# Optimization experiments

Hardware: AMD Instinct MI355X
Metric: run time of the kernel (lower is better)

The kernel has to match this reference:

```python
import jax, jax.numpy as jnp
import numpy as np

B, N, DEG = 64, 512, 16        # graphs, nodes per graph, avg degree
C, HID = 10, 128               # input feat dim (== num_classes quirk), hidden
E = B * N * DEG                # total edges (fixed; pooling masks edges)


def _gcn(x, W, b, src, dst, emask, n):
    # PyG GCNConv: add self-loops, symmetric norm D^-1/2 (A+I) D^-1/2 (XW) + b
    h = x @ W
    deg = jax.ops.segment_sum(emask, dst, num_segments=n) + 1.0  # +1 self-loop
    dinv = jax.lax.rsqrt(deg)
    norm = dinv[src] * dinv[dst] * emask
    agg = jax.ops.segment_sum(h[src] * norm[:, None], dst, num_segments=n)
    return agg + h * (dinv * dinv)[:, None] + b  # self-loop term + bias


def _sag_pool(x, src, dst, emask, Wp, bp, n_per):
    # SAGPooling: score = tanh(GCN(x)); per-graph top-k (ratio=0.5); x' = x[perm]*score
    n = x.shape[0]
    score = jnp.tanh(_gcn(x, Wp, bp, src, dst, emask, n)[:, 0])
    k = n_per // 2
    vals, idx = jax.lax.top_k(score.reshape(B, n_per), k)  # [B,k]
    perm = (idx + (jnp.arange(B) * n_per)[:, None]).reshape(-1)
    xk = x[perm] * vals.reshape(-1)[:, None]
    # relabel edges; drop edges touching removed nodes via mask (fixed E)
    mapping = jnp.full((n,), -1, jnp.int32).at[perm].set(
        jnp.arange(B * k, dtype=jnp.int32))
    ns, nd = mapping[src], mapping[dst]
    nmask = emask * ((ns >= 0) & (nd >= 0)).astype(emask.dtype)
    return xk, jnp.maximum(ns, 0), jnp.maximum(nd, 0), nmask, k


def _readout(x, k):
    # global max pool || global mean pool (all kept nodes are real, no padding)
    xg = x.reshape(B, k, -1)
    return jnp.concatenate([xg.max(axis=1), xg.mean(axis=1)], axis=1)


def setup_inputs() -> dict:
    key = jax.random.key(0)
    ks = jax.random.split(key, 16)
    x = jax.random.normal(ks[0], (B * N, C), jnp.float32)
    off = jnp.repeat(jnp.arange(B, dtype=jnp.int32) * N, N * DEG)
    src = jax.random.randint(ks[1], (E,), 0, N, jnp.int32) + off
    dst = jax.random.randint(ks[2], (E,), 0, N, jnp.int32) + off
    p = lambda k, s: jax.random.normal(k, s, jnp.float32) * 0.05
    return {
        "x": x, "src": src, "dst": dst,
        "W1": p(ks[3], (C, HID)), "b1": jnp.zeros((HID,), jnp.float32),
        "W2": p(ks[4], (HID, HID)), "b2": jnp.zeros((HID,), jnp.float32),
        "W3": p(ks[5], (HID, HID)), "b3": jnp.zeros((HID,), jnp.float32),
        "Wp": p(ks[6], (HID, 1)), "bp": jnp.zeros((1,), jnp.float32),
        "L1W": p(ks[7], (2 * HID, HID)), "L1b": jnp.zeros((HID,), jnp.float32),
        "L2W": p(ks[8], (HID, HID // 2)), "L2b": jnp.zeros((HID // 2,), jnp.float32),
    }


def reference(x, src, dst, W1, b1, W2, b2, W3, b3, Wp, bp, L1W, L1b, L2W, L2b):
    emask = jnp.ones((E,), jnp.float32)
    h = jax.nn.relu(_gcn(x, W1, b1, src, dst, emask, B * N))
    h, src, dst, emask, k = _sag_pool(h, src, dst, emask, Wp, bp, N)
    x1 = _readout(h, k)
    h = jax.nn.relu(_gcn(h, W2, b2, src, dst, emask, B * k))
    h, src, dst, emask, k = _sag_pool(h, src, dst, emask, Wp, bp, k)
    x2 = _readout(h, k)
    h = jax.nn.relu(_gcn(h, W3, b3, src, dst, emask, B * k))
    h, src, dst, emask, k = _sag_pool(h, src, dst, emask, Wp, bp, k)
    x3 = _readout(h, k)
    z = x1 + x2 + x3
    z = jax.nn.relu(z @ L1W + L1b)
    # dropout inactive in eval mode
    z = jax.nn.relu(z @ L2W + L2b)
    return jax.nn.log_softmax(z, axis=1)
```

## Files before the change

### kernel.cpp

```cpp
#include <hip/hip_runtime.h>
#include <math.h>

#define BGR 64
#define N0 512
#define E_TOT (BGR*N0*16)
#define EPG 8192
#define EIT 16
#define HID 128


__global__ __launch_bounds__(512) void k_topo0(
    const int* __restrict__ s0, const int* __restrict__ d0,
    int2* __restrict__ edges, int* __restrict__ cnt, int* __restrict__ rowptr,
    float* __restrict__ dinv, int2* __restrict__ csr){
  __shared__ int   deg[512];
  __shared__ int   sb[512];
  __shared__ int   cur[512];
  __shared__ float dl[512];
  int g = (blockIdx.x & 7)*8 + (blockIdx.x >> 3);
  int t = threadIdx.x;
  int gbase = g*N0, ebase = g*EPG;
  deg[t] = 0;
  __syncthreads();
  int2 ebuf[EIT];
  #pragma unroll
  for (int it = 0; it < EIT; it++){
    int i = ebase + it*512 + t;
    int2 e = make_int2(s0[i], d0[i]);
    ebuf[it] = e;
    edges[i] = e;
    atomicAdd(&deg[e.y - gbase], 1);
  }
  __syncthreads();
  int vdeg = deg[t];
  sb[t] = vdeg; __syncthreads();
  for (int off = 1; off < 512; off <<= 1){
    int add = (t >= off) ? sb[t-off] : 0;
    __syncthreads(); sb[t] += add; __syncthreads();
  }
  int excl = sb[t] - vdeg;
  rowptr[gbase + t] = ebase + excl;
  cnt[gbase + t] = vdeg;
  cur[t] = excl;
  float dv = rsqrtf((float)vdeg + 1.f);
  dl[t] = dv;
  dinv[gbase + t] = dv;
  __syncthreads();
  #pragma unroll
  for (int it = 0; it < EIT; it++){
    int2 e = ebuf[it];
    int sl = e.x - gbase, dc = e.y - gbase;
    int pos = atomicAdd(&cur[dc], 1);
    csr[ebase + pos] = make_int2(e.x, __float_as_int(dl[sl]*dl[dc]));
  }
}

__global__ __launch_bounds__(512) void k_l1_fused(
    const float* __restrict__ x, const float* __restrict__ W1,
    const int2* __restrict__ csr, const int* __restrict__ rowptr,
    const int* __restrict__ cnt, const float* __restrict__ dinv,
    const float* __restrict__ b1, const float* __restrict__ Wp,
    float4* __restrict__ gout4, float* __restrict__ hp_part){
  extern __shared__ float hl[];
  int b = blockIdx.x;
  int xcd = b & 7, idx = b >> 3;
  int graph = xcd*8 + (idx >> 3);
  int sub = idx & 7;
  int qf = sub >> 1, half = sub & 1;
  int t = threadIdx.x;
  int gbase = graph*N0;
  int fp = t & 31;
  int f = qf*32 + fp;
  float wcol[10];
  #pragma unroll
  for (int k = 0; k < 10; k++) wcol[k] = W1[k*HID + f];
  for (int n = t >> 5; n < N0; n += 16){
    const float* xr = x + (gbase + n)*10;
    float acc = 0.f;
    #pragma unroll
    for (int k = 0; k < 10; k++) acc += xr[k]*wcol[k];
    hl[n*32 + fp] = acc;
  }
  __syncthreads();
  const float4* hl4 = (const float4*)hl;
  int l = t & 7, grp = t >> 3;
  float4 bb = ((const float4*)b1)[qf*8 + l];
  float4 wp = ((const float4*)Wp)[qf*8 + l];
  int n0 = half*256;
  for (int nl = n0 + grp; nl < n0 + 256; nl += 64){
    int node = gbase + nl;
    int start = rowptr[node], c = cnt[node];
    float4 acc = make_float4(0.f,0.f,0.f,0.f);
    int j = 0;
    for (; j + 4 <= c; j += 4){
      int2 e0 = csr[start+j],   e1 = csr[start+j+1];
      int2 e2 = csr[start+j+2], e3 = csr[start+j+3];
      float4 h0 = hl4[(e0.x - gbase)*8 + l];
      float4 h1 = hl4[(e1.x - gbase)*8 + l];
      float4 h2 = hl4[(e2.x - gbase)*8 + l];
      float4 h3 = hl4[(e3.x - gbase)*8 + l];
      float w0 = __int_as_float(e0.y), w1 = __int_as_float(e1.y);
      float w2 = __int_as_float(e2.y), w3 = __int_as_float(e3.y);
      acc.x += w0*h0.x + w1*h1.x + w2*h2.x + w3*h3.x;
      acc.y += w0*h0.y + w1*h1.y + w2*h2.y + w3*h3.y;
      acc.z += w0*h0.z + w1*h1.z + w2*h2.z + w3*h3.z;
      acc.w += w0*h0.w + w1*h1.w + w2*h2.w + w3*h3.w;
    }
    for (; j < c; j++){
      int2 e = csr[start + j];
      float wgt = __int_as_float(e.y);
      float4 hv = hl4[(e.x - gbase)*8 + l];
      acc.x += wgt*hv.x; acc.y += wgt*hv.y; acc.z += wgt*hv.z; acc.w += wgt*hv.w;
    }
    float di = dinv[node], dd = di*di;
    float4 hs = hl4[nl*8 + l];
    float4 v;
    v.x = fmaxf(acc.x + hs.x*dd + bb.x, 0.f);
    v.y = fmaxf(acc.y + hs.y*dd + bb.y, 0.f);
    v.z = fmaxf(acc.z + hs.z*dd + bb.z, 0.f);
    v.w = fmaxf(acc.w + hs.w*dd + bb.w, 0.f);
    gout4[node*32 + qf*8 + l] = v;
    float contrib = v.x*wp.x + v.y*wp.y + v.z*wp.z + v.w*wp.w;
    #pragma unroll
    for (int off = 4; off; off >>= 1) contrib += __shfl_down(contrib, off, 8);
    if (l == 0) hp_part[qf*32768 + node] = contrib;
  }
}

__global__ void k_gemm16(const float* __restrict__ x, const float* __restrict__ W,
                         float* __restrict__ out, int nper){
  __shared__ float xr[16][HID];
  int b = blockIdx.x;
  int xcd = b & 7, idx = b >> 3, bpg = nper >> 4;
  int graph = xcd*8 + idx / bpg;
  int base = graph*nper + (idx % bpg)*16;
  int f = threadIdx.x;
  #pragma unroll
  for (int nd = 0; nd < 16; nd++) xr[nd][f] = x[(base+nd)*HID + f];
  __syncthreads();
  float acc[16];
  #pragma unroll
  for (int nd = 0; nd < 16; nd++) acc[nd] = 0.f;
  for (int i = 0; i < HID; i++){
    float wv = W[i*HID + f];
    #pragma unroll
    for (int nd = 0; nd < 16; nd++) acc[nd] += xr[nd][i]*wv;
  }
  #pragma unroll
  for (int nd = 0; nd < 16; nd++) out[(base+nd)*HID + f] = acc[nd];
}

__global__ __launch_bounds__(256) void k_gcn_gather(
    const float4* __restrict__ h4, const int2* __restrict__ csr,
    const int* __restrict__ rowptr, const int* __restrict__ cnt,
    const float* __restrict__ dinv, const float4* __restrict__ bias4,
    const float4* __restrict__ Wp4, float4* __restrict__ out4,
    float* __restrict__ hp, int nper){
  int b = blockIdx.x;
  int xcd = b & 7, idx = b >> 3, bpg = nper >> 3;
  int graph = xcd*8 + idx / bpg;
  int node = graph*nper + (idx % bpg)*8 + (threadIdx.x >> 5);
  int l = threadIdx.x & 31;
  int start = rowptr[node], c = cnt[node];
  float4 acc = make_float4(0.f, 0.f, 0.f, 0.f);
  int j = 0;
  for (; j + 4 <= c; j += 4){
    int2 e0 = csr[start+j],   e1 = csr[start+j+1];
    int2 e2 = csr[start+j+2], e3 = csr[start+j+3];
    float4 h0 = h4[e0.x*32 + l];
    float4 h1 = h4[e1.x*32 + l];
    float4 h2 = h4[e2.x*32 + l];
    float4 h3 = h4[e3.x*32 + l];
    float w0 = __int_as_float(e0.y), w1 = __int_as_float(e1.y);
    float w2 = __int_as_float(e2.y), w3 = __int_as_float(e3.y);
    acc.x += w0*h0.x + w1*h1.x + w2*h2.x + w3*h3.x;
    acc.y += w0*h0.y + w1*h1.y + w2*h2.y + w3*h3.y;
    acc.z += w0*h0.z + w1*h1.z + w2*h2.z + w3*h3.z;
    acc.w += w0*h0.w + w1*h1.w + w2*h2.w + w3*h3.w;
  }
  for (; j < c; j++){
    int2 e = csr[start + j];
    float wgt = __int_as_float(e.y);
    float4 hv = h4[e.x*32 + l];
    acc.x += wgt*hv.x; acc.y += wgt*hv.y; acc.z += wgt*hv.z; acc.w += wgt*hv.w;
  }
  float di = dinv[node], dd = di*di;
  float4 hs = h4[node*32 + l];
  float4 bb = bias4[l];
  float4 v;
  v.x = fmaxf(acc.x + hs.x*dd + bb.x, 0.f);
  v.y = fmaxf(acc.y + hs.y*dd + bb.y, 0.f);
  v.z = fmaxf(acc.z + hs.z*dd + bb.z, 0.f);
  v.w = fmaxf(acc.w + hs.w*dd + bb.w, 0.f);
  out4[node*32 + l] = v;
  float4 wp = Wp4[l];
  float contrib = v.x*wp.x + v.y*wp.y + v.z*wp.z + v.w*wp.w;
  #pragma unroll
  for (int off = 16; off; off >>= 1) contrib += __shfl_down(contrib, off, 32);
  if (l == 0) hp[node] = contrib;
}

__global__ __launch_bounds__(512) void k_mega(
    const float4* __restrict__ gout4, const float* __restrict__ hp_part,
    int l1flag, const float* __restrict__ hp,
    int2* __restrict__ csr, int* __restrict__ rowptr, int* __restrict__ cnt,
    float* __restrict__ dinv, const float* __restrict__ bp,
    int2* __restrict__ edges, float4* __restrict__ xpool4,
    float* __restrict__ z, int nper, int lastlev,
    const float* __restrict__ L1W, const float* __restrict__ L1b,
    const float* __restrict__ L2W, const float* __restrict__ L2b,
    float* __restrict__ out){
  __shared__ float sv[512];
  __shared__ int   si[512];
  __shared__ float hpl[512];
  __shared__ int   map[512];
  __shared__ int   sb[512];
  __shared__ int   cur[256];
  __shared__ float dl[256];
  __shared__ float4 pmx[16][32];
  __shared__ float4 psm[16][32];
  __shared__ float zr[256];
  __shared__ float h1[128];
  __shared__ float h2[64];
  __shared__ float red[2];
  int g = (blockIdx.x & 7)*8 + (blockIdx.x >> 3);
  int t = threadIdx.x;
  int k = nper >> 1;
  int gbase = g*nper, ebase = g*EPG, gb2 = g*k;
  bool act = t < nper;
  if (act){
    int node = gbase + t;
    hpl[t] = l1flag ? (hp_part[node] + hp_part[32768 + node] +
                       hp_part[65536 + node] + hp_part[98304 + node])
                    : hp[node];
  }
  __syncthreads();
  float v = 0.f; int idx = t;
  if (act){
    int start = rowptr[gbase + t], c = cnt[gbase + t];
    float a = 0.f;
    int j = 0;
    for (; j + 4 <= c; j += 4){
      int2 e0 = csr[start+j],   e1 = csr[start+j+1];
      int2 e2 = csr[start+j+2], e3 = csr[start+j+3];
      a += __int_as_float(e0.y)*hpl[e0.x - gbase]
         + __int_as_float(e1.y)*hpl[e1.x - gbase]
         + __int_as_float(e2.y)*hpl[e2.x - gbase]
         + __int_as_float(e3.y)*hpl[e3.x - gbase];
    }
    for (; j < c; j++){
      int2 e = csr[start + j];
      a += __int_as_float(e.y)*hpl[e.x - gbase];
    }
    float di = dinv[gbase + t];
    v = tanhf(a + hpl[t]*di*di + bp[0]);
  }
  for (int kk = 2; kk <= nper; kk <<= 1){
    for (int jj = kk >> 1; jj > 0; jj >>= 1){
      if (jj >= 64){
        if (act){ sv[t] = v; si[t] = idx; }
        __syncthreads();
        if (act){
          int p = t ^ jj;
          float pv = sv[p]; int pi = si[p];
          bool amLower = (t & jj) == 0;
          bool dirDesc = (t & kk) == 0;
          bool betterMine = (v > pv) || (v == pv && idx < pi);
          if ((amLower == dirDesc) != betterMine){ v = pv; idx = pi; }
        }
        __syncthreads();
      } else if (act){
        float pv = __shfl_xor(v, jj);
        int   pi = __shfl_xor(idx, jj);
        bool amLower = (t & jj) == 0;
        bool dirDesc = (t & kk) == 0;
        bool betterMine = (v > pv) || (v == pv && idx < pi);
        if ((amLower == dirDesc) != betterMine){ v = pv; idx = pi; }
      }
    }
  }
  if (act){ sv[t] = v; si[t] = idx; }
  __syncthreads();
  int l = t & 31, j0 = t >> 5;
  float4 mx = make_float4(-INFINITY,-INFINITY,-INFINITY,-INFINITY);
  float4 sm = make_float4(0.f,0.f,0.f,0.f);
  for (int j = j0; j < k; j += 16){
    float val = sv[j]; int row = si[j];
    float4 hv = gout4[(gbase + row)*32 + l];
    float4 o = make_float4(hv.x*val, hv.y*val, hv.z*val, hv.w*val);
    if (!lastlev) xpool4[(gb2 + j)*32 + l] = o;
    mx.x = fmaxf(mx.x, o.x); mx.y = fmaxf(mx.y, o.y);
    mx.z = fmaxf(mx.z, o.z); mx.w = fmaxf(mx.w, o.w);
    sm.x += o.x; sm.y += o.y; sm.z += o.z; sm.w += o.w;
  }
  pmx[j0][l] = mx; psm[j0][l] = sm;
  __syncthreads();
  if (t < 32){
    float4 M = pmx[0][t], S = psm[0][t];
    #pragma unroll
    for (int q = 1; q < 16; q++){
      float4 m2 = pmx[q][t], s2 = psm[q][t];
      M.x = fmaxf(M.x, m2.x); M.y = fmaxf(M.y, m2.y);
      M.z = fmaxf(M.z, m2.z); M.w = fmaxf(M.w, m2.w);
      S.x += s2.x; S.y += s2.y; S.z += s2.z; S.w += s2.w;
    }
    float ki = 1.f/(float)k;
    float* zp = z + g*256;
    if (l1flag){
      zp[t*4+0] = M.x; zp[t*4+1] = M.y; zp[t*4+2] = M.z; zp[t*4+3] = M.w;
      zp[128+t*4+0] = S.x*ki; zp[128+t*4+1] = S.y*ki;
      zp[128+t*4+2] = S.z*ki; zp[128+t*4+3] = S.w*ki;
    } else if (!lastlev){
      zp[t*4+0] += M.x; zp[t*4+1] += M.y; zp[t*4+2] += M.z; zp[t*4+3] += M.w;
      zp[128+t*4+0] += S.x*ki; zp[128+t*4+1] += S.y*ki;
      zp[128+t*4+2] += S.z*ki; zp[128+t*4+3] += S.w*ki;
    } else {
      zr[t*4+0] = zp[t*4+0] + M.x; zr[t*4+1] = zp[t*4+1] + M.y;
      zr[t*4+2] = zp[t*4+2] + M.z; zr[t*4+3] = zp[t*4+3] + M.w;
      zr[128+t*4+0] = zp[128+t*4+0] + S.x*ki;
      zr[128+t*4+1] = zp[128+t*4+1] + S.y*ki;
      zr[128+t*4+2] = zp[128+t*4+2] + S.z*ki;
      zr[128+t*4+3] = zp[128+t*4+3] + S.w*ki;
    }
  }
  if (lastlev){
    __syncthreads();
    if (t < 128){
      float a = L1b[t];
      for (int i = 0; i < 256; i++) a += zr[i]*L1W[i*128 + t];
      h1[t] = fmaxf(a, 0.f);
    }
    __syncthreads();
    if (t < 64){
      float a = L2b[t];
      for (int i = 0; i < 128; i++) a += h1[i]*L2W[i*64 + t];
      h2[t] = fmaxf(a, 0.f);
    }
    __syncthreads();
    if (t == 0){
      float mxv = -INFINITY;
      for (int i = 0; i < 64; i++) mxv = fmaxf(mxv, h2[i]);
      float s = 0.f;
      for (int i = 0; i < 64; i++) s += expf(h2[i] - mxv);
      red[0] = mxv; red[1] = logf(s);
    }
    __syncthreads();
    if (t < 64) out[g*64 + t] = h2[t] - red[0] - red[1];
    return;
  }
  if (act) map[t] = -1;
  if (t < k) sb[t] = 0;
  __syncthreads();
  if (t < k) map[si[t]] = t;
  __syncthreads();
  int2 ebuf[EIT];
  #pragma unroll
  for (int it = 0; it < EIT; it++){
    int i = ebase + it*512 + t;
    int2 e = edges[i];
    int2 ne = make_int2(-1, 0);
    if (e.x >= 0){
      int ns = map[e.x - gbase], nd = map[e.y - gbase];
      if (ns >= 0 && nd >= 0){
        ne = make_int2(gb2 + ns, gb2 + nd);
        atomicAdd(&sb[nd], 1);
      }
    }
    ebuf[it] = ne;
    edges[i] = ne;
  }
  __syncthreads();
  int vdeg = (t < k) ? sb[t] : 0;
  for (int off = 1; off < k; off <<= 1){
    int add = (t >= off && t < k) ? sb[t-off] : 0;
    __syncthreads();
    if (t < k) sb[t] += add;
    __syncthreads();
  }
  if (t < k){
    int excl = sb[t] - vdeg;
    rowptr[gb2 + t] = ebase + excl;
    cnt[gb2 + t] = vdeg;
    cur[t] = excl;
    float dv = rsqrtf((float)vdeg + 1.f);
    dl[t] = dv;
    dinv[gb2 + t] = dv;
  }
  __syncthreads();
  #pragma unroll
  for (int it = 0; it < EIT; it++){
    int2 e = ebuf[it];
    if (e.x >= 0){
      int sl = e.x - gb2, dc = e.y - gb2;
      int pos = atomicAdd(&cur[dc], 1);
      csr[ebase + pos] = make_int2(e.x, __float_as_int(dl[sl]*dl[dc]));
    }
  }
}

extern "C" void kernel_launch(void* const* d_in, const int* in_sizes, int n_in,
                              void* d_out, int out_size, void* d_ws, size_t ws_size,
                              hipStream_t stream){
  (void)in_sizes; (void)n_in; (void)out_size; (void)ws_size;
  const float* x0  = (const float*)d_in[0];
  const int*   s0  = (const int*)  d_in[1];
  const int*   d0  = (const int*)  d_in[2];
  const float* W1  = (const float*)d_in[3];  const float* b1 = (const float*)d_in[4];
  const float* W2  = (const float*)d_in[5];  const float* b2 = (const float*)d_in[6];
  const float* W3  = (const float*)d_in[7];  const float* b3 = (const float*)d_in[8];
  const float* Wp  = (const float*)d_in[9];  const float* bp = (const float*)d_in[10];
  const float* L1W = (const float*)d_in[11]; const float* L1b = (const float*)d_in[12];
  const float* L2W = (const float*)d_in[13]; const float* L2b = (const float*)d_in[14];
  float* out = (float*)d_out;

  float* w = (float*)d_ws;
  float* h     = w; w += 32768*HID;
  float* gout  = w; w += 32768*HID;
  float* xpA   = h    + 16384*HID;
  float* xpB   = gout + 16384*HID;
  float* xpC   = xpA;
  float* dinvv = w; w += 32768;
  float* hp    = w; w += 32768;
  float* hppt  = w; w += 4*32768;
  float* z     = w; w += BGR*256;
  int* cnt     = (int*)w; w += 32768;
  int* rowptr  = (int*)w; w += 32768;
  int2* edges  = (int2*)w; w += 2*E_TOT;
  int2* csr    = (int2*)w; w += 2*E_TOT;

  k_topo0<<<BGR, 512, 0, stream>>>(s0, d0, edges, cnt, rowptr, dinvv, csr);

  k_l1_fused<<<512, 512, 65536, stream>>>(x0, W1, csr, rowptr, cnt, dinvv,
                                          b1, Wp, (float4*)gout, hppt);
  k_mega<<<BGR, 512, 0, stream>>>((const float4*)gout, hppt, 1, hp, csr, rowptr,
                                  cnt, dinvv, bp, edges, (float4*)xpA, z, 512, 0,
                                  L1W, L1b, L2W, L2b, out);
  k_gemm16<<<16384/16, HID, 0, stream>>>(xpA, W2, h, 256);
  k_gcn_gather<<<16384/8, 256, 0, stream>>>((const float4*)h, csr, rowptr, cnt,
                                            dinvv, (const float4*)b2,
                                            (const float4*)Wp, (float4*)gout,
                                            hp, 256);
  k_mega<<<BGR, 512, 0, stream>>>((const float4*)gout, hppt, 0, hp, csr, rowptr,
                                  cnt, dinvv, bp, edges, (float4*)xpB, z, 256, 0,
                                  L1W, L1b, L2W, L2b, out);
  k_gemm16<<<8192/16, HID, 0, stream>>>(xpB, W3, h, 128);
  k_gcn_gather<<<8192/8, 256, 0, stream>>>((const float4*)h, csr, rowptr, cnt,
                                           dinvv, (const float4*)b3,
                                           (const float4*)Wp, (float4*)gout,
                                           hp, 128);
  k_mega<<<BGR, 512, 0, stream>>>((const float4*)gout, hppt, 0, hp, csr, rowptr,
                                  cnt, dinvv, bp, edges, (float4*)xpC, z, 128, 1,
                                  L1W, L1b, L2W, L2b, out);
}
```

Before: 246.0 us.

## Fuse pooled gather into GEMM, widen mega kernel, use wave-shuffle scans

The pooling kernel no longer writes the scaled pooled feature matrix. It stores only the selected indices and scores, and the following GEMM gathers rows from the previous layer's output and scales them as it loads. The mega kernel now runs 1024 threads per graph, splitting the score aggregation across several threads per node, and uses twice as many threads for the edge relabel. Both LDS Hillis-Steele prefix scans (topology and relabel) become wave-level shuffle scans with per-wave sums, which cuts barriers. The trade-offs are indirect, less coalesced loads in the GEMM and heavier register and LDS pressure from the larger blocks.

```diff
diff --git a/kernel.cpp b/kernel.cpp
--- a/kernel.cpp
+++ b/kernel.cpp
@@ -14,9 +14,9 @@
     int2* __restrict__ edges, int* __restrict__ cnt, int* __restrict__ rowptr,
     float* __restrict__ dinv, int2* __restrict__ csr){
   __shared__ int   deg[512];
-  __shared__ int   sb[512];
   __shared__ int   cur[512];
   __shared__ float dl[512];
+  __shared__ int   wsum[8];
   int g = (blockIdx.x & 7)*8 + (blockIdx.x >> 3);
   int t = threadIdx.x;
   int gbase = g*N0, ebase = g*EPG;
@@ -33,12 +33,19 @@
   }
   __syncthreads();
   int vdeg = deg[t];
-  sb[t] = vdeg; __syncthreads();
-  for (int off = 1; off < 512; off <<= 1){
-    int add = (t >= off) ? sb[t-off] : 0;
-    __syncthreads(); sb[t] += add; __syncthreads();
-  }
-  int excl = sb[t] - vdeg;
+  int lane = t & 63, wid = t >> 6;
+  int x = vdeg;
+  #pragma unroll
+  for (int off = 1; off < 64; off <<= 1){
+    int y = __shfl_up(x, off);
+    if (lane >= off) x += y;
+  }
+  if (lane == 63) wsum[wid] = x;
+  __syncthreads();
+  int prefix = 0;
+  #pragma unroll
+  for (int wj = 0; wj < 8; wj++) prefix += (wj < wid) ? wsum[wj] : 0;
+  int excl = x + prefix - vdeg;
   rowptr[gbase + t] = ebase + excl;
   cnt[gbase + t] = vdeg;
   cur[t] = excl;
@@ -127,16 +134,23 @@
   }
 }
 
-__global__ void k_gemm16(const float* __restrict__ x, const float* __restrict__ W,
-                         float* __restrict__ out, int nper){
+__global__ void k_gemm16p(const float* __restrict__ gprev,
+                          const int* __restrict__ sig,
+                          const float* __restrict__ svg,
+                          const float* __restrict__ W,
+                          float* __restrict__ out, int nprev, int nper){
   __shared__ float xr[16][HID];
   int b = blockIdx.x;
   int xcd = b & 7, idx = b >> 3, bpg = nper >> 4;
   int graph = xcd*8 + idx / bpg;
-  int base = graph*nper + (idx % bpg)*16;
+  int lb = (idx % bpg)*16;
   int f = threadIdx.x;
   #pragma unroll
-  for (int nd = 0; nd < 16; nd++) xr[nd][f] = x[(base+nd)*HID + f];
+  for (int nd = 0; nd < 16; nd++){
+    int row  = sig[graph*512 + lb + nd];
+    float val = svg[graph*512 + lb + nd];
+    xr[nd][f] = gprev[(graph*nprev + row)*HID + f] * val;
+  }
   __syncthreads();
   float acc[16];
   #pragma unroll
@@ -147,7 +161,7 @@
     for (int nd = 0; nd < 16; nd++) acc[nd] += xr[nd][i]*wv;
   }
   #pragma unroll
-  for (int nd = 0; nd < 16; nd++) out[(base+nd)*HID + f] = acc[nd];
+  for (int nd = 0; nd < 16; nd++) out[(graph*nper + lb + nd)*HID + f] = acc[nd];
 }
 
 __global__ __launch_bounds__(256) void k_gcn_gather(
@@ -200,12 +214,12 @@
   if (l == 0) hp[node] = contrib;
 }
 
-__global__ __launch_bounds__(512) void k_mega(
+__global__ __launch_bounds__(1024) void k_mega(
     const float4* __restrict__ gout4, const float* __restrict__ hp_part,
     int l1flag, const float* __restrict__ hp,
     int2* __restrict__ csr, int* __restrict__ rowptr, int* __restrict__ cnt,
     float* __restrict__ dinv, const float* __restrict__ bp,
-    int2* __restrict__ edges, float4* __restrict__ xpool4,
+    int2* __restrict__ edges, int* __restrict__ sig, float* __restrict__ svg,
     float* __restrict__ z, int nper, int lastlev,
     const float* __restrict__ L1W, const float* __restrict__ L1b,
     const float* __restrict__ L2W, const float* __restrict__ L2b,
@@ -213,10 +227,12 @@
   __shared__ float sv[512];
   __shared__ int   si[512];
   __shared__ float hpl[512];
-  __shared__ int   map[512];
+  __shared__ float spart[1024];
+  __shared__ int   map_[512];
   __shared__ int   sb[512];
   __shared__ int   cur[256];
   __shared__ float dl[256];
+  __shared__ int   wsum[4];
   __shared__ float4 pmx[16][32];
   __shared__ float4 psm[16][32];
   __shared__ float zr[256];
@@ -227,7 +243,10 @@
   int t = threadIdx.x;
   int k = nper >> 1;
   int gbase = g*nper, ebase = g*EPG, gb2 = g*k;
+  int SPL = 1024/nper;
+  int n = t & (nper-1), p = t / nper;
   bool act = t < nper;
+
   if (act){
     int node = gbase + t;
     hpl[t] = l1flag ? (hp_part[node] + hp_part[32768 + node] +
@@ -235,23 +254,21 @@
                     : hp[node];
   }
   __syncthreads();
+  {
+    int start = rowptr[gbase + n], c = cnt[gbase + n];
+    int lo = (c*p)/SPL, hi = (c*(p+1))/SPL;
+    float a = 0.f;
+    for (int j = lo; j < hi; j++){
+      int2 e = csr[start + j];
+      a += __int_as_float(e.y)*hpl[e.x - gbase];
+    }
+    spart[t] = a;
+  }
+  __syncthreads();
   float v = 0.f; int idx = t;
   if (act){
-    int start = rowptr[gbase + t], c = cnt[gbase + t];
     float a = 0.f;
-    int j = 0;
-    for (; j + 4 <= c; j += 4){
-      int2 e0 = csr[start+j],   e1 = csr[start+j+1];
-      int2 e2 = csr[start+j+2], e3 = csr[start+j+3];
-      a += __int_as_float(e0.y)*hpl[e0.x - gbase]
-         + __int_as_float(e1.y)*hpl[e1.x - gbase]
-         + __int_as_float(e2.y)*hpl[e2.x - gbase]
-         + __int_as_float(e3.y)*hpl[e3.x - gbase];
-    }
-    for (; j < c; j++){
-      int2 e = csr[start + j];
-      a += __int_as_float(e.y)*hpl[e.x - gbase];
-    }
+    for (int pp = 0; pp < SPL; pp++) a += spart[t + pp*nper];
     float di = dinv[gbase + t];
     v = tanhf(a + hpl[t]*di*di + bp[0]);
   }
@@ -261,8 +278,8 @@
         if (act){ sv[t] = v; si[t] = idx; }
         __syncthreads();
         if (act){
-          int p = t ^ jj;
-          float pv = sv[p]; int pi = si[p];
+          int pr = t ^ jj;
+          float pv = sv[pr]; int pi = si[pr];
           bool amLower = (t & jj) == 0;
           bool dirDesc = (t & kk) == 0;
           bool betterMine = (v > pv) || (v == pv && idx < pi);
@@ -282,18 +299,20 @@
   if (act){ sv[t] = v; si[t] = idx; }
   __syncthreads();
   int l = t & 31, j0 = t >> 5;
-  float4 mx = make_float4(-INFINITY,-INFINITY,-INFINITY,-INFINITY);
-  float4 sm = make_float4(0.f,0.f,0.f,0.f);
-  for (int j = j0; j < k; j += 16){
-    float val = sv[j]; int row = si[j];
-    float4 hv = gout4[(gbase + row)*32 + l];
-    float4 o = make_float4(hv.x*val, hv.y*val, hv.z*val, hv.w*val);
-    if (!lastlev) xpool4[(gb2 + j)*32 + l] = o;
-    mx.x = fmaxf(mx.x, o.x); mx.y = fmaxf(mx.y, o.y);
-    mx.z = fmaxf(mx.z, o.z); mx.w = fmaxf(mx.w, o.w);
-    sm.x += o.x; sm.y += o.y; sm.z += o.z; sm.w += o.w;
-  }
-  pmx[j0][l] = mx; psm[j0][l] = sm;
+  if (t < 512){
+    float4 mx = make_float4(-INFINITY,-INFINITY,-INFINITY,-INFINITY);
+    float4 sm = make_float4(0.f,0.f,0.f,0.f);
+    for (int j = j0; j < k; j += 16){
+      float val = sv[j]; int row = si[j];
+      float4 hv = gout4[(gbase + row)*32 + l];
+      float4 o = make_float4(hv.x*val, hv.y*val, hv.z*val, hv.w*val);
+      mx.x = fmaxf(mx.x, o.x); mx.y = fmaxf(mx.y, o.y);
+      mx.z = fmaxf(mx.z, o.z); mx.w = fmaxf(mx.w, o.w);
+      sm.x += o.x; sm.y += o.y; sm.z += o.z; sm.w += o.w;
+    }
+    pmx[j0][l] = mx; psm[j0][l] = sm;
+  }
+  if (t < 512 && t < k && !lastlev){ sig[g*512 + t] = si[t]; svg[g*512 + t] = sv[t]; }
   __syncthreads();
   if (t < 32){
     float4 M = pmx[0][t], S = psm[0][t];
@@ -348,19 +367,19 @@
     if (t < 64) out[g*64 + t] = h2[t] - red[0] - red[1];
     return;
   }
-  if (act) map[t] = -1;
+  if (act) map_[t] = -1;
   if (t < k) sb[t] = 0;
   __syncthreads();
-  if (t < k) map[si[t]] = t;
-  __syncthreads();
-  int2 ebuf[EIT];
-  #pragma unroll
-  for (int it = 0; it < EIT; it++){
-    int i = ebase + it*512 + t;
+  if (t < k) map_[si[t]] = t;
+  __syncthreads();
+  int2 ebuf[8];
+  #pragma unroll
+  for (int it = 0; it < 8; it++){
+    int i = ebase + it*1024 + t;
     int2 e = edges[i];
     int2 ne = make_int2(-1, 0);
     if (e.x >= 0){
-      int ns = map[e.x - gbase], nd = map[e.y - gbase];
+      int ns = map_[e.x - gbase], nd = map_[e.y - gbase];
       if (ns >= 0 && nd >= 0){
         ne = make_int2(gb2 + ns, gb2 + nd);
         atomicAdd(&sb[nd], 1);
@@ -371,14 +390,20 @@
   }
   __syncthreads();
   int vdeg = (t < k) ? sb[t] : 0;
-  for (int off = 1; off < k; off <<= 1){
-    int add = (t >= off && t < k) ? sb[t-off] : 0;
-    __syncthreads();
-    if (t < k) sb[t] += add;
-    __syncthreads();
-  }
+  int lane = t & 63, wid = t >> 6;
+  int x = vdeg;
+  #pragma unroll
+  for (int off = 1; off < 64; off <<= 1){
+    int y = __shfl_up(x, off);
+    if (lane >= off) x += y;
+  }
+  if (t < k && lane == 63) wsum[wid] = x;
+  __syncthreads();
   if (t < k){
-    int excl = sb[t] - vdeg;
+    int prefix = 0;
+    #pragma unroll
+    for (int wj = 0; wj < 4; wj++) prefix += (wj < wid) ? wsum[wj] : 0;
+    int excl = x + prefix - vdeg;
     rowptr[gb2 + t] = ebase + excl;
     cnt[gb2 + t] = vdeg;
     cur[t] = excl;
@@ -388,7 +413,7 @@
   }
   __syncthreads();
   #pragma unroll
-  for (int it = 0; it < EIT; it++){
+  for (int it = 0; it < 8; it++){
     int2 e = ebuf[it];
     if (e.x >= 0){
       int sl = e.x - gb2, dc = e.y - gb2;
@@ -416,13 +441,12 @@
   float* w = (float*)d_ws;
   float* h     = w; w += 32768*HID;
   float* gout  = w; w += 32768*HID;
-  float* xpA   = h    + 16384*HID;
-  float* xpB   = gout + 16384*HID;
-  float* xpC   = xpA;
   float* dinvv = w; w += 32768;
   float* hp    = w; w += 32768;
   float* hppt  = w; w += 4*32768;
   float* z     = w; w += BGR*256;
+  float* svg   = w; w += 32768;
+  int* sig     = (int*)w; w += 32768;
   int* cnt     = (int*)w; w += 32768;
   int* rowptr  = (int*)w; w += 32768;
   int2* edges  = (int2*)w; w += 2*E_TOT;
@@ -432,23 +456,23 @@
 
   k_l1_fused<<<512, 512, 65536, stream>>>(x0, W1, csr, rowptr, cnt, dinvv,
                                           b1, Wp, (float4*)gout, hppt);
-  k_mega<<<BGR, 512, 0, stream>>>((const float4*)gout, hppt, 1, hp, csr, rowptr,
-                                  cnt, dinvv, bp, edges, (float4*)xpA, z, 512, 0,
-                                  L1W, L1b, L2W, L2b, out);
-  k_gemm16<<<16384/16, HID, 0, stream>>>(xpA, W2, h, 256);
+  k_mega<<<BGR, 1024, 0, stream>>>((const float4*)gout, hppt, 1, hp, csr,
+                                   rowptr, cnt, dinvv, bp, edges, sig, svg,
+                                   z, 512, 0, L1W, L1b, L2W, L2b, out);
+  k_gemm16p<<<16384/16, HID, 0, stream>>>(gout, sig, svg, W2, h, 512, 256);
   k_gcn_gather<<<16384/8, 256, 0, stream>>>((const float4*)h, csr, rowptr, cnt,
                                             dinvv, (const float4*)b2,
                                             (const float4*)Wp, (float4*)gout,
                                             hp, 256);
-  k_mega<<<BGR, 512, 0, stream>>>((const float4*)gout, hppt, 0, hp, csr, rowptr,
-                                  cnt, dinvv, bp, edges, (float4*)xpB, z, 256, 0,
-                                  L1W, L1b, L2W, L2b, out);
-  k_gemm16<<<8192/16, HID, 0, stream>>>(xpB, W3, h, 128);
+  k_mega<<<BGR, 1024, 0, stream>>>((const float4*)gout, hppt, 0, hp, csr,
+                                   rowptr, cnt, dinvv, bp, edges, sig, svg,
+                                   z, 256, 0, L1W, L1b, L2W, L2b, out);
+  k_gemm16p<<<8192/16, HID, 0, stream>>>(gout, sig, svg, W3, h, 256, 128);
   k_gcn_gather<<<8192/8, 256, 0, stream>>>((const float4*)h, csr, rowptr, cnt,
                                            dinvv, (const float4*)b3,
                                            (const float4*)Wp, (float4*)gout,
                                            hp, 128);
-  k_mega<<<BGR, 512, 0, stream>>>((const float4*)gout, hppt, 0, hp, csr, rowptr,
-                                  cnt, dinvv, bp, edges, (float4*)xpC, z, 128, 1,
-                                  L1W, L1b, L2W, L2b, out);
-}
+  k_mega<<<BGR, 1024, 0, stream>>>((const float4*)gout, hppt, 0, hp, csr,
+                                   rowptr, cnt, dinvv, bp, edges, sig, svg,
+                                   z, 128, 1, L1W, L1b, L2W, L2b, out);
+}
```

Result: no change. 243.0 us (-1.2%).
